# Optimization experiments

Hardware: AMD Instinct MI355X
Metric: run time of the kernel (lower is better)

The kernel has to match this reference:

```python
import jax, jax.numpy as jnp
import numpy as np

N_GRAPHS = 200
NODES_PER_GRAPH = 500
N_NODES = N_GRAPHS * NODES_PER_GRAPH  # 100000
N_EDGES = 1_600_000
INPUT_DIM = 64
GCN_DIM = 128
SEQ_LEN = 20
LSTM_DIM = 128
OUTPUT_DIM = 1


def setup_inputs() -> dict:
    key = jax.random.key(0)
    ks = jax.random.split(key, 10)
    # edges constrained to stay inside each graph (block-diagonal adjacency)
    src = jax.random.randint(ks[0], (N_EDGES,), 0, N_NODES, dtype=jnp.int32)
    dst_local = jax.random.randint(ks[1], (N_EDGES,), 0, NODES_PER_GRAPH, dtype=jnp.int32)
    dst = (src // NODES_PER_GRAPH) * NODES_PER_GRAPH + dst_local
    graph_ids = jnp.arange(N_NODES, dtype=jnp.int32) // NODES_PER_GRAPH
    x = jax.random.normal(ks[2], (N_NODES, INPUT_DIM), dtype=jnp.float32)
    s = 0.05
    w_gcn = jax.random.normal(ks[3], (INPUT_DIM, GCN_DIM), dtype=jnp.float32) * s
    b_gcn = jnp.zeros((GCN_DIM,), dtype=jnp.float32)
    w_ih = jax.random.normal(ks[4], (4 * LSTM_DIM, GCN_DIM), dtype=jnp.float32) * s
    w_hh = jax.random.normal(ks[5], (4 * LSTM_DIM, LSTM_DIM), dtype=jnp.float32) * s
    b_ih = jax.random.normal(ks[6], (4 * LSTM_DIM,), dtype=jnp.float32) * s
    b_hh = jax.random.normal(ks[7], (4 * LSTM_DIM,), dtype=jnp.float32) * s
    w_fc = jax.random.normal(ks[8], (OUTPUT_DIM, LSTM_DIM), dtype=jnp.float32) * s
    b_fc = jnp.zeros((OUTPUT_DIM,), dtype=jnp.float32)
    return {"x": x, "src": src, "dst": dst, "graph_ids": graph_ids,
            "w_gcn": w_gcn, "b_gcn": b_gcn, "w_ih": w_ih, "w_hh": w_hh,
            "b_ih": b_ih, "b_hh": b_hh, "w_fc": w_fc, "b_fc": b_fc}


def reference(x, src, dst, graph_ids, w_gcn, b_gcn, w_ih, w_hh, b_ih, b_hh, w_fc, b_fc):
    ones_e = jnp.ones((src.shape[0],), dtype=x.dtype)
    # DGL GraphConv norm='both': D_out^{-1/2} on src side, D_in^{-1/2} on dst side,
    # degrees clamped to min 1 (allow_zero_in_degree=True)
    out_deg = jnp.clip(jax.ops.segment_sum(ones_e, src, num_segments=N_NODES), 1.0)
    in_deg = jnp.clip(jax.ops.segment_sum(ones_e, dst, num_segments=N_NODES), 1.0)
    h = x * (out_deg ** -0.5)[:, None]                               # [N, Din]
    agg = jax.ops.segment_sum(h[src], dst, num_segments=N_NODES)     # gather+scatter-add
    h = agg * (in_deg ** -0.5)[:, None]
    h = jnp.maximum(h @ w_gcn + b_gcn, 0.0)                           # [N, GCN_DIM], ReLU
    # dgl.mean_nodes: per-graph mean pool
    cnt = jax.ops.segment_sum(jnp.ones((N_NODES,), h.dtype), graph_ids, num_segments=N_GRAPHS)
    hg = jax.ops.segment_sum(h, graph_ids, num_segments=N_GRAPHS) / cnt[:, None]  # [T, D]
    # build_dataset: sliding windows of length SEQ_LEN over the graph time series
    B = N_GRAPHS - SEQ_LEN + 1
    idx = jnp.arange(B)[:, None] + jnp.arange(SEQ_LEN)[None, :]
    dat = hg[idx]                                                      # [B, L, D]
    # single-layer LSTM (PyTorch gate order i,f,g,o), zero initial state
    x_proj = jnp.einsum('bld,gd->blg', dat, w_ih) + b_ih               # [B, L, 4H]
    h0 = jnp.zeros((B, LSTM_DIM), dat.dtype)
    c0 = jnp.zeros((B, LSTM_DIM), dat.dtype)

    def step(carry, xt):
        hprev, cprev = carry
        gates = xt + hprev @ w_hh.T + b_hh
        i, f, g, o = jnp.split(gates, 4, axis=-1)
        c = jax.nn.sigmoid(f) * cprev + jax.nn.sigmoid(i) * jnp.tanh(g)
        hh = jax.nn.sigmoid(o) * jnp.tanh(c)
        return (hh, c), None

    (h_n, _), _ = jax.lax.scan(step, (h0, c0), jnp.swapaxes(x_proj, 0, 1))
    pred = h_n @ w_fc.T + b_fc                                         # [B, OUTPUT_DIM]
    return pred
```

## Files before the change

### kernel.cpp

```cpp
#include <hip/hip_runtime.h>
#include <hip/hip_bf16.h>

#define N_GRAPHS 200
#define NPG      500
#define N_NODES_ 100000
#define N_EDGES_ 1600000
#define DIN      64
#define DG       128
#define SEQ      20
#define HL       128
#define G4       512
#define BWIN     (N_GRAPHS - SEQ + 1)
#define NPART    256
#define EPB      (N_EDGES_/NPART)
#define CELL     80
#define CPG      (NPART*CELL)
#define SCAP     10752

typedef __attribute__((ext_vector_type(8))) short short8;
typedef __attribute__((ext_vector_type(4))) float float4v;
typedef __attribute__((ext_vector_type(2))) float floatx2;
typedef __attribute__((ext_vector_type(2))) _Float16 half2v;

__device__ __forceinline__ float sigmoidf_(float v){ return 1.0f/(1.0f+__expf(-v)); }
__device__ __forceinline__ float tanhf_(float x){
  float e = __expf(2.0f*x);
  return 1.0f - 2.0f/(e + 1.0f);
}

__device__ __forceinline__ unsigned short f2bf(float f) {
  unsigned int u = __float_as_uint(f);
  u += 0x7fffu + ((u >> 16) & 1u);
  return (unsigned short)(u >> 16);
}

__device__ __forceinline__ float h2dot(half2v a, half2v b, float c) {
#if __has_builtin(__builtin_amdgcn_fdot2)
  return __builtin_amdgcn_fdot2(a, b, c, false);
#else
  return c + (float)a.x*(float)b.x + (float)a.y*(float)b.y;
#endif
}

__global__ __launch_bounds__(1024) void k_part(const int* __restrict__ src,
                                               const int* __restrict__ dst,
                                               const float* __restrict__ w_hh,
                                               int* __restrict__ part,
                                               int* __restrict__ pcnt,
                                               int4* __restrict__ whh16) {
  __shared__ int cnt[N_GRAPHS];
  __shared__ int buf[N_GRAPHS][CELL];
  int b = blockIdx.x, t = threadIdx.x;
  if (b < 8) {
    int i = b*1024 + t;
    int k4 = i >> 9, r = i & 511;
    const float4* wp = (const float4*)(w_hh + (size_t)r*HL + k4*8);
    float4 w0 = wp[0], w1 = wp[1];
    half2v p0 = {(_Float16)w0.x, (_Float16)w0.y};
    half2v p1 = {(_Float16)w0.z, (_Float16)w0.w};
    half2v p2 = {(_Float16)w1.x, (_Float16)w1.y};
    half2v p3 = {(_Float16)w1.z, (_Float16)w1.w};
    int4 pk;
    pk.x = __builtin_bit_cast(int, p0); pk.y = __builtin_bit_cast(int, p1);
    pk.z = __builtin_bit_cast(int, p2); pk.w = __builtin_bit_cast(int, p3);
    whh16[i] = pk;
  }
  if (t < N_GRAPHS) cnt[t] = 0;
  __syncthreads();
  int e0 = b*EPB;
  const int2* s2 = (const int2*)(src + e0);
  const int2* d2 = (const int2*)(dst + e0);
  for (int i = t; i < EPB/2; i += 1024) {
    int2 ss = s2[i], dd = d2[i];
    {
      int g = ss.x / NPG;
      int pk = ((ss.x - g*NPG) << 9) | (dd.x - g*NPG);
      int pos = atomicAdd(&cnt[g], 1);
      if (pos < CELL) buf[g][pos] = pk;
    }
    {
      int g = ss.y / NPG;
      int pk = ((ss.y - g*NPG) << 9) | (dd.y - g*NPG);
      int pos = atomicAdd(&cnt[g], 1);
      if (pos < CELL) buf[g][pos] = pk;
    }
  }
  __syncthreads();
  int w = t >> 6, lane = t & 63;
  for (int g = w; g < N_GRAPHS; g += 16) {
    int n = min(cnt[g], CELL);
    int ba = g*CPG + b*CELL;
    if (lane < n)      part[ba + lane]      = buf[g][lane];
    if (lane + 64 < n) part[ba + lane + 64] = buf[g][lane + 64];
  }
  if (t < N_GRAPHS) pcnt[t*NPART + b] = min(cnt[t], CELL);
}

__global__ __launch_bounds__(1024, 4) void k_graph(
    const int* __restrict__ pcnt, const int* __restrict__ part,
    const float* __restrict__ x,
    const float* __restrict__ w_gcn, const float* __restrict__ b_gcn,
    const float* __restrict__ w_ih,  const float* __restrict__ b_ih,
    float* __restrict__ proj) {
  __shared__ int meta[2048];
  __shared__ int ccnt[256], coff[256];
  __shared__ int wsum[8], wsum4[4];
  __shared__ int qhead, nsegS;
  __shared__ __align__(16) float hgS[DG];
  __shared__ unsigned short sorted[SCAP];
  __shared__ __align__(16) int4 xs[4008];
  __shared__ __align__(16) int4 hpre[4096];
  int* indeg  = meta;
  int* outdeg = meta + 512;
  int* off    = meta + 1024;
  float* soS  = (float*)(meta + 1536);
  int* eC     = (int*)xs;
  int g = blockIdx.x, t = threadIdx.x;
  int lane = t & 63, w = t >> 6;

  const float4* xg = ((const float4*)x) + (size_t)g*8000;
  float4 xr[8];
  #pragma unroll
  for (int q = 0; q < 8; ++q) {
    int i = t + q*1024;
    if (i < 8000) xr[q] = xg[i];
  }
  float4 wg[2];
  #pragma unroll
  for (int q = 0; q < 2; ++q) wg[q] = ((const float4*)w_gcn)[t + q*1024];

  meta[t] = 0; meta[t + 1024] = 0;
  int cv = 0, csc = 0;
  if (t < 256) {
    cv = pcnt[g*NPART + t];
    ccnt[t] = cv;
    csc = cv;
    #pragma unroll
    for (int o = 1; o < 64; o <<= 1) { int nn = __shfl_up(csc, o); if (lane >= o) csc += nn; }
    if (lane == 63) wsum4[w] = csc;
  }
  __syncthreads();
  if (t < 256) {
    int woff = 0;
    #pragma unroll
    for (int i = 0; i < 4; ++i) woff += (i < w) ? wsum4[i] : 0;
    coff[t] = woff + csc - cv;
    if (t == 255) nsegS = woff + csc;
  }
  __syncthreads();
  #pragma unroll
  for (int it = 0; it < 20; ++it) {
    int slot = it*1024 + t;
    unsigned cell = (unsigned)slot / CELL;
    int k = slot - (int)cell*CELL;
    if (k < ccnt[cell]) {
      int p = part[(size_t)g*CPG + slot];
      eC[coff[cell] + k] = p;
      atomicAdd(&indeg[p & 511], 1);
      atomicAdd(&outdeg[p >> 9], 1);
    }
  }
  __syncthreads();
  int vscan = 0, v4 = 0, scscan = 0;
  if (t < 512) {
    vscan = indeg[t];
    v4 = (vscan + 3) & ~3;
    scscan = v4;
    #pragma unroll
    for (int o = 1; o < 64; o <<= 1) { int nn = __shfl_up(scscan, o); if (lane >= o) scscan += nn; }
    if (lane == 63) wsum[w] = scscan;
  }
  __syncthreads();
  if (t < 512) {
    int woff = 0;
    #pragma unroll
    for (int i = 0; i < 8; ++i) woff += (i < w) ? wsum[i] : 0;
    off[t] = woff + scscan - v4;
    soS[t] = rsqrtf((float)max(outdeg[t], 1));
  }
  if (t == 0) qhead = 128;
  __syncthreads();
  int nseg = nsegS;
  for (int e = t; e < nseg; e += 1024) {
    int p = eC[e];
    int pos = atomicAdd(&off[p & 511], 1);
    sorted[pos] = (unsigned short)(p >> 9);
  }
  __syncthreads();
  if (t < 512) {
    int e = off[t], ee = (e + 3) & ~3;
    for (; e < ee; ++e) sorted[e] = 500;
  }
  ushort4* xd = (ushort4*)xs;
  #pragma unroll
  for (int q = 0; q < 8; ++q) {
    int i = t + q*1024;
    if (i < 8000) {
      float4 vv = xr[q];
      float s2 = soS[i >> 4];
      ushort4 u;
      u.x = f2bf(vv.x*s2); u.y = f2bf(vv.y*s2); u.z = f2bf(vv.z*s2); u.w = f2bf(vv.w*s2);
      xd[i] = u;
    }
  }
  if (t < 16) xd[8000 + t] = make_ushort4(0,0,0,0);
  __syncthreads();
  int g8 = lane >> 3, fl = lane & 7;
  int nl = w*8 + g8;
  while (nl < 512) {
    int4 outv = make_int4(0,0,0,0);
    if (nl < NPG) {
      int end = off[nl], dgr = indeg[nl], st = end - dgr;
      floatx2 a0 = {0.f,0.f}, a1 = {0.f,0.f}, a2 = {0.f,0.f}, a3 = {0.f,0.f};
      for (int c0 = 0; c0 < dgr; c0 += 4) {
        ushort4 e4 = *(const ushort4*)(sorted + st + c0);
        #pragma unroll
        for (int j = 0; j < 4; ++j) {
          int se = (j==0) ? e4.x : (j==1) ? e4.y : (j==2) ? e4.z : e4.w;
          int4 vv = xs[(se << 3) + fl];
          floatx2 u0 = { __uint_as_float((unsigned)vv.x & 0xffff0000u),
                         __uint_as_float((unsigned)vv.x << 16) };
          floatx2 u1 = { __uint_as_float((unsigned)vv.y & 0xffff0000u),
                         __uint_as_float((unsigned)vv.y << 16) };
          floatx2 u2 = { __uint_as_float((unsigned)vv.z & 0xffff0000u),
                         __uint_as_float((unsigned)vv.z << 16) };
          floatx2 u3 = { __uint_as_float((unsigned)vv.w & 0xffff0000u),
                         __uint_as_float((unsigned)vv.w << 16) };
          a0 += u0; a1 += u1; a2 += u2; a3 += u3;
        }
      }
      float sn = rsqrtf((float)max(dgr, 1));
      outv.x = (int)(((unsigned)f2bf(a0.y*sn)) | ((unsigned)f2bf(a0.x*sn) << 16));
      outv.y = (int)(((unsigned)f2bf(a1.y*sn)) | ((unsigned)f2bf(a1.x*sn) << 16));
      outv.z = (int)(((unsigned)f2bf(a2.y*sn)) | ((unsigned)f2bf(a2.x*sn) << 16));
      outv.w = (int)(((unsigned)f2bf(a3.y*sn)) | ((unsigned)f2bf(a3.x*sn) << 16));
    }
    hpre[(nl << 3) + (fl ^ (nl & 7))] = outv;
    int nxt = 0;
    if (fl == 0) nxt = atomicAdd(&qhead, 1);
    nl = __shfl(nxt, (g8 << 3));
  }
  __syncthreads();
  unsigned short* wLds = (unsigned short*)sorted;
  #pragma unroll
  for (int q = 0; q < 2; ++q) {
    int i = t + q*1024;
    int k = i >> 5, c4 = (i & 31) << 2;
    int h = k >> 5, j = k & 7, lhi = ((k >> 3) & 3) << 4;
    float vvv[4] = {wg[q].x, wg[q].y, wg[q].z, wg[q].w};
    #pragma unroll
    for (int u = 0; u < 4; ++u) {
      int n = c4 + u;
      int idx = ((n >> 4)*2 + h)*64 + lhi + (n & 15);
      wLds[idx*8 + j] = f2bf(vvv[u]);
    }
  }
  __syncthreads();
  float* pS = (float*)meta;
  int quad = lane >> 4, l15 = lane & 15;
  float bcol[8];
  #pragma unroll
  for (int nt = 0; nt < 8; ++nt) bcol[nt] = b_gcn[nt*16 + l15];
  float psum[8] = {0.f,0.f,0.f,0.f,0.f,0.f,0.f,0.f};
  #pragma unroll
  for (int i = 0; i < 2; ++i) {
    int row0 = (w + 16*i) << 4;
    int r = row0 + l15;
    int4 a0i = hpre[(r << 3) + (quad ^ (r & 7))];
    int4 a1i = hpre[(r << 3) + ((quad + 4) ^ (r & 7))];
    short8 a0 = *(const short8*)&a0i;
    short8 a1 = *(const short8*)&a1i;
    #pragma unroll
    for (int nt = 0; nt < 8; ++nt) {
      short8 b0 = *((const short8*)&wLds[((nt*2+0)*64 + lane)*8]);
      short8 b1 = *((const short8*)&wLds[((nt*2+1)*64 + lane)*8]);
      float4v acc = {0.f, 0.f, 0.f, 0.f};
      acc = __builtin_amdgcn_mfma_f32_16x16x32_bf16(a0, b0, acc, 0, 0, 0);
      acc = __builtin_amdgcn_mfma_f32_16x16x32_bf16(a1, b1, acc, 0, 0, 0);
      #pragma unroll
      for (int r4 = 0; r4 < 4; ++r4) {
        int node = row0 + quad*4 + r4;
        float vvv = acc[r4] + bcol[nt];
        psum[nt] += (node < NPG) ? fmaxf(vvv, 0.f) : 0.f;
      }
    }
  }
  #pragma unroll
  for (int nt = 0; nt < 8; ++nt) {
    float vvv = psum[nt];
    vvv += __shfl_xor(vvv, 16);
    vvv += __shfl_xor(vvv, 32);
    if (lane < 16) pS[w*DG + nt*16 + lane] = vvv;
  }
  __syncthreads();
  if (t < DG) {
    float sum = 0.f;
    #pragma unroll
    for (int w16 = 0; w16 < 16; ++w16) sum += pS[w16*DG + t];
    hgS[t] = sum * (1.0f/NPG);
  }
  __syncthreads();
  {
    int r = t >> 1, half = t & 1;
    const float4* wr = (const float4*)(w_ih + (size_t)r*HL) + half*16;
    const float4* hv = (const float4*)hgS + half*16;
    float acc = half ? 0.f : b_ih[r];
    #pragma unroll
    for (int k4 = 0; k4 < 16; ++k4) {
      float4 w4 = wr[k4]; float4 h4 = hv[k4];
      acc += w4.x*h4.x + w4.y*h4.y + w4.z*h4.z + w4.w*h4.w;
    }
    acc += __shfl_xor(acc, 1);
    if (!half) proj[(size_t)g*G4 + r] = acc;
  }
}

__global__ __launch_bounds__(512, 2) void k_lstm(const float* __restrict__ proj,
    const int4* __restrict__ whh16, const float* __restrict__ b_hh,
    const float* __restrict__ w_fc, const float* __restrict__ b_fc,
    float* __restrict__ out) {
  __shared__ __align__(16) int4 hA[16], hB[16];
  __shared__ float fcS[8];
  int b = blockIdx.x, t = threadIdx.x;
  int e = t >> 2, q = t & 3;
  int r = q*HL + e;
  float pj[SEQ];
  #pragma unroll
  for (int l = 0; l < SEQ; ++l) pj[l] = proj[(size_t)(b+l)*G4 + r];
  int4 W[16];
  #pragma unroll
  for (int k4 = 0; k4 < 16; ++k4) W[k4] = whh16[(k4 << 9) + r];
  if (t < 16) hA[t] = make_int4(0,0,0,0);
  float bh = b_hh[r];
  float wfc = w_fc[e];
  float c = 0.f;
  __syncthreads();
  #pragma unroll
  for (int l = 0; l < SEQ; ++l) {
    const int4* Rb = (l & 1) ? hB : hA;
    int*       Wb = (int*)((l & 1) ? hA : hB);
    float a0 = pj[l] + bh;
    float a1 = 0.f, a2 = 0.f, a3 = 0.f;
    #pragma unroll
    for (int k4 = 0; k4 < 16; k4 += 4) {
      int4 hv0 = Rb[k4+0]; int4 hv1 = Rb[k4+1];
      int4 hv2 = Rb[k4+2]; int4 hv3 = Rb[k4+3];
      a0 = h2dot(__builtin_bit_cast(half2v, W[k4+0].x), __builtin_bit_cast(half2v, hv0.x), a0);
      a0 = h2dot(__builtin_bit_cast(half2v, W[k4+0].y), __builtin_bit_cast(half2v, hv0.y), a0);
      a0 = h2dot(__builtin_bit_cast(half2v, W[k4+0].z), __builtin_bit_cast(half2v, hv0.z), a0);
      a0 = h2dot(__builtin_bit_cast(half2v, W[k4+0].w), __builtin_bit_cast(half2v, hv0.w), a0);
      a1 = h2dot(__builtin_bit_cast(half2v, W[k4+1].x), __builtin_bit_cast(half2v, hv1.x), a1);
      a1 = h2dot(__builtin_bit_cast(half2v, W[k4+1].y), __builtin_bit_cast(half2v, hv1.y), a1);
      a1 = h2dot(__builtin_bit_cast(half2v, W[k4+1].z), __builtin_bit_cast(half2v, hv1.z), a1);
      a1 = h2dot(__builtin_bit_cast(half2v, W[k4+1].w), __builtin_bit_cast(half2v, hv1.w), a1);
      a2 = h2dot(__builtin_bit_cast(half2v, W[k4+2].x), __builtin_bit_cast(half2v, hv2.x), a2);
      a2 = h2dot(__builtin_bit_cast(half2v, W[k4+2].y), __builtin_bit_cast(half2v, hv2.y), a2);
      a2 = h2dot(__builtin_bit_cast(half2v, W[k4+2].z), __builtin_bit_cast(half2v, hv2.z), a2);
      a2 = h2dot(__builtin_bit_cast(half2v, W[k4+2].w), __builtin_bit_cast(half2v, hv2.w), a2);
      a3 = h2dot(__builtin_bit_cast(half2v, W[k4+3].x), __builtin_bit_cast(half2v, hv3.x), a3);
      a3 = h2dot(__builtin_bit_cast(half2v, W[k4+3].y), __builtin_bit_cast(half2v, hv3.y), a3);
      a3 = h2dot(__builtin_bit_cast(half2v, W[k4+3].z), __builtin_bit_cast(half2v, hv3.z), a3);
      a3 = h2dot(__builtin_bit_cast(half2v, W[k4+3].w), __builtin_bit_cast(half2v, hv3.w), a3);
    }
    float v = (a0 + a1) + (a2 + a3);
    int base = t & ~3;
    float iv = __shfl(v, base+0);
    float fv = __shfl(v, base+1);
    float gv = __shfl(v, base+2);
    float ov = __shfl(v, base+3);
    float h = 0.f;
    if (q == 0) {
      iv = sigmoidf_(iv); fv = sigmoidf_(fv);
      gv = tanhf_(gv);    ov = sigmoidf_(ov);
      c = fv*c + iv*gv;
      h = ov * tanhf_(c);
    }
    float hRight = __shfl(h, (t & ~7) + 4);
    if ((t & 7) == 0) {
      half2v hp = {(_Float16)h, (_Float16)hRight};
      Wb[e >> 1] = __builtin_bit_cast(int, hp);
    }
    if (l == SEQ-1) {
      float s = (q == 0) ? h * wfc : 0.f;
      #pragma unroll
      for (int o = 32; o > 0; o >>= 1) s += __shfl_down(s, o);
      if ((t & 63) == 0) fcS[t >> 6] = s;
    }
    __syncthreads();
  }
  if (t == 0) {
    float s = 0.f;
    #pragma unroll
    for (int i = 0; i < 8; ++i) s += fcS[i];
    out[b] = s + b_fc[0];
  }
}

extern "C" void kernel_launch(void* const* d_in, const int* in_sizes, int n_in,
                              void* d_out, int out_size, void* d_ws, size_t ws_size,
                              hipStream_t stream) {
  const float* x     = (const float*)d_in[0];
  const int*   src   = (const int*)d_in[1];
  const int*   dst   = (const int*)d_in[2];
  const float* w_gcn = (const float*)d_in[4];
  const float* b_gcn = (const float*)d_in[5];
  const float* w_ih  = (const float*)d_in[6];
  const float* w_hh  = (const float*)d_in[7];
  const float* b_ih  = (const float*)d_in[8];
  const float* b_hh  = (const float*)d_in[9];
  const float* w_fc  = (const float*)d_in[10];
  const float* b_fc  = (const float*)d_in[11];
  float* out = (float*)d_out;

  char* ws = (char*)d_ws;
  size_t off = 0;
  auto alloc = [&](size_t bytes) -> void* {
    void* p = ws + off; off += (bytes + 255) & ~(size_t)255; return p;
  };
  int* part    = (int*)alloc((size_t)N_GRAPHS*CPG*4);
  int* pcnt    = (int*)alloc((size_t)N_GRAPHS*NPART*4);
  int4* whh16  = (int4*)alloc((size_t)8192*16);
  float* proj  = (float*)alloc((size_t)N_GRAPHS*G4*4);
  (void)ws_size; (void)in_sizes; (void)n_in; (void)out_size;

  k_part<<<NPART, 1024, 0, stream>>>(src, dst, w_hh, part, pcnt, whh16);
  k_graph<<<N_GRAPHS, 1024, 0, stream>>>(pcnt, part, x, w_gcn, b_gcn, w_ih, b_ih, proj);
  k_lstm<<<BWIN, 512, 0, stream>>>(proj, whh16, b_hh, w_fc, b_fc, out);
}
```

Measured before the change: 159.6 us.

## Exchange LSTM gates through shared memory instead of shuffles in k_lstm

Each thread now computes the gate row equal to its thread index and writes it to a shared gate array. After a barrier, 128 threads apply the nonlinearities, update the cell state and write the packed fp16 hidden state into a single shared buffer. This removes the four cross-lane shuffles and the predicated gate math spread across all 512 threads. In exchange it adds a second __syncthreads per timestep, drops the hidden-state double buffer, and relaxes the launch bound from two blocks per CU to one.

```diff
diff --git a/kernel.cpp b/kernel.cpp
--- a/kernel.cpp
+++ b/kernel.cpp
@@ -315,36 +315,32 @@
   }
 }
 
-__global__ __launch_bounds__(512, 2) void k_lstm(const float* __restrict__ proj,
+__global__ __launch_bounds__(512) void k_lstm(const float* __restrict__ proj,
     const int4* __restrict__ whh16, const float* __restrict__ b_hh,
     const float* __restrict__ w_fc, const float* __restrict__ b_fc,
     float* __restrict__ out) {
-  __shared__ __align__(16) int4 hA[16], hB[16];
-  __shared__ float fcS[8];
+  __shared__ float gS[G4];
+  __shared__ __align__(16) int4 hPi[16];
+  __shared__ float fcS[2];
   int b = blockIdx.x, t = threadIdx.x;
-  int e = t >> 2, q = t & 3;
-  int r = q*HL + e;
   float pj[SEQ];
   #pragma unroll
-  for (int l = 0; l < SEQ; ++l) pj[l] = proj[(size_t)(b+l)*G4 + r];
+  for (int l = 0; l < SEQ; ++l) pj[l] = proj[(size_t)(b+l)*G4 + t];
   int4 W[16];
   #pragma unroll
-  for (int k4 = 0; k4 < 16; ++k4) W[k4] = whh16[(k4 << 9) + r];
-  if (t < 16) hA[t] = make_int4(0,0,0,0);
-  float bh = b_hh[r];
-  float wfc = w_fc[e];
+  for (int k4 = 0; k4 < 16; ++k4) W[k4] = whh16[(k4 << 9) + t];
+  if (t < 16) hPi[t] = make_int4(0,0,0,0);
+  float bh = b_hh[t];
   float c = 0.f;
   __syncthreads();
   #pragma unroll
   for (int l = 0; l < SEQ; ++l) {
-    const int4* Rb = (l & 1) ? hB : hA;
-    int*       Wb = (int*)((l & 1) ? hA : hB);
     float a0 = pj[l] + bh;
     float a1 = 0.f, a2 = 0.f, a3 = 0.f;
     #pragma unroll
     for (int k4 = 0; k4 < 16; k4 += 4) {
-      int4 hv0 = Rb[k4+0]; int4 hv1 = Rb[k4+1];
-      int4 hv2 = Rb[k4+2]; int4 hv3 = Rb[k4+3];
+      int4 hv0 = hPi[k4+0]; int4 hv1 = hPi[k4+1];
+      int4 hv2 = hPi[k4+2]; int4 hv3 = hPi[k4+3];
       a0 = h2dot(__builtin_bit_cast(half2v, W[k4+0].x), __builtin_bit_cast(half2v, hv0.x), a0);
       a0 = h2dot(__builtin_bit_cast(half2v, W[k4+0].y), __builtin_bit_cast(half2v, hv0.y), a0);
       a0 = h2dot(__builtin_bit_cast(half2v, W[k4+0].z), __builtin_bit_cast(half2v, hv0.z), a0);
@@ -362,38 +358,30 @@
       a3 = h2dot(__builtin_bit_cast(half2v, W[k4+3].z), __builtin_bit_cast(half2v, hv3.z), a3);
       a3 = h2dot(__builtin_bit_cast(half2v, W[k4+3].w), __builtin_bit_cast(half2v, hv3.w), a3);
     }
-    float v = (a0 + a1) + (a2 + a3);
-    int base = t & ~3;
-    float iv = __shfl(v, base+0);
-    float fv = __shfl(v, base+1);
-    float gv = __shfl(v, base+2);
-    float ov = __shfl(v, base+3);
-    float h = 0.f;
-    if (q == 0) {
-      iv = sigmoidf_(iv); fv = sigmoidf_(fv);
-      gv = tanhf_(gv);    ov = sigmoidf_(ov);
+    gS[t] = (a0 + a1) + (a2 + a3);
+    __syncthreads();
+    if (t < 128) {
+      float iv = sigmoidf_(gS[t]);
+      float fv = sigmoidf_(gS[HL + t]);
+      float gv = tanhf_(gS[2*HL + t]);
+      float ov = sigmoidf_(gS[3*HL + t]);
       c = fv*c + iv*gv;
-      h = ov * tanhf_(c);
-    }
-    float hRight = __shfl(h, (t & ~7) + 4);
-    if ((t & 7) == 0) {
-      half2v hp = {(_Float16)h, (_Float16)hRight};
-      Wb[e >> 1] = __builtin_bit_cast(int, hp);
-    }
-    if (l == SEQ-1) {
-      float s = (q == 0) ? h * wfc : 0.f;
-      #pragma unroll
-      for (int o = 32; o > 0; o >>= 1) s += __shfl_down(s, o);
-      if ((t & 63) == 0) fcS[t >> 6] = s;
+      float h = ov * tanhf_(c);
+      float hp2 = __shfl_xor(h, 1);
+      if (!(t & 1)) {
+        half2v hp = {(_Float16)h, (_Float16)hp2};
+        ((int*)hPi)[t >> 1] = __builtin_bit_cast(int, hp);
+      }
+      if (l == SEQ-1) {
+        float s = h * w_fc[t];
+        #pragma unroll
+        for (int o = 32; o > 0; o >>= 1) s += __shfl_down(s, o);
+        if ((t & 63) == 0) fcS[t >> 6] = s;
+      }
     }
     __syncthreads();
   }
-  if (t == 0) {
-    float s = 0.f;
-    #pragma unroll
-    for (int i = 0; i < 8; ++i) s += fcS[i];
-    out[b] = s + b_fc[0];
-  }
+  if (t == 0) out[b] = fcS[0] + fcS[1] + b_fc[0];
 }
 
 extern "C" void kernel_launch(void* const* d_in, const int* in_sizes, int n_in,
```

Measured after the change: 155.4 us. 2.7% less time.
